# Kernel tuning notes

Hardware: AMD Instinct MI355X
Metric: run time of the kernel (lower is better)

The kernel has to match this reference:

```python
import jax, jax.numpy as jnp
import numpy as np

IN_DIM = 3
N_FEATS = 8
HASHMAP_SIZE = 524288
RESOLUTION = 128.0
PRIMES = np.array([1, 2654435761, 805459861], dtype=np.uint32)
# bin_mask[n, d] = (n & (1 << d)) == 0, for the 2^d corner offsets
_neigh = np.arange(1 << IN_DIM, dtype=np.int64).reshape(-1, 1)
_dims = np.arange(IN_DIM, dtype=np.int64).reshape(1, -1)
BIN_MASK = (_neigh & (1 << _dims)) == 0  # [8, 3] bool


def setup_inputs() -> dict:
    key = jax.random.key(0)
    k1, k2 = jax.random.split(key)
    x = jax.random.uniform(k1, (2000000, IN_DIM), dtype=jnp.float32)
    emb = jax.random.normal(k2, (HASHMAP_SIZE, N_FEATS), dtype=jnp.float32) * 0.1
    return {"x": x, "emb": emb}


def _hash(idx_u32, primes_u32):
    # idx_u32: [..., d] uint32; multiply wraps mod 2^32 (== & 0xFFFFFFFF), xor-reduce dims
    p = idx_u32 * primes_u32  # uint32 wraparound
    h = p[..., 0]
    for i in range(1, p.shape[-1]):
        h = h ^ p[..., i]
    return (h % jnp.uint32(HASHMAP_SIZE)).astype(jnp.int32)


def reference(x, emb):
    primes = jnp.asarray(PRIMES)
    bin_mask = jnp.asarray(BIN_MASK)  # [8, 3]
    xr = x * RESOLUTION                      # [N, 3]
    xi = jnp.floor(xr)                       # [N, 3] float (long() on positive coords)
    xf = xr - xi                             # fractional part; grad == identity (detach on xi)
    xi_u = xi.astype(jnp.uint32)
    # corner integer coords: [N, 8, 3]
    idx = jnp.where(bin_mask[None, :, :], xi_u[:, None, :], xi_u[:, None, :] + jnp.uint32(1))
    # trilinear weights: [N, 8]
    w = jnp.prod(jnp.where(bin_mask[None, :, :], 1.0 - xf[:, None, :], xf[:, None, :]), axis=-1)
    hash_ids = _hash(idx, primes)            # [N, 8] int32
    feats = emb[hash_ids]                    # [N, 8, F]
    return jnp.sum(feats * w[..., None], axis=-2)  # [N, F]
```

## Files before the change

kernel.cpp:

```cpp
#include <hip/hip_runtime.h>


#define HASHMAP_SIZE 524288
#define HASHMAP_MASK 524287u
#define RESOLUTION   128.0f
#define PRIME1       2654435761u
#define PRIME2       805459861u

typedef float f32x4 __attribute__((ext_vector_type(4)));
typedef int   i32x2 __attribute__((ext_vector_type(2)));
typedef int   i32x4 __attribute__((ext_vector_type(4)));

#define NRED_BLOCKS 256

__global__ __launch_bounds__(256) void absmax_stage1(
    const float* __restrict__ emb, float* __restrict__ blockmax)
{
    __shared__ float smax[256];
    int tid = threadIdx.x;
    int stride = gridDim.x * blockDim.x;
    const float4* e4 = reinterpret_cast<const float4*>(emb);
    const int total4 = HASHMAP_SIZE * 2;
    float m = 0.f;
    for (int idx = blockIdx.x * blockDim.x + tid; idx < total4; idx += stride) {
        float4 v = e4[idx];
        m = fmaxf(m, fmaxf(fmaxf(fabsf(v.x), fabsf(v.y)),
                           fmaxf(fabsf(v.z), fabsf(v.w))));
    }
    smax[tid] = m;
    __syncthreads();
    for (int s = 128; s > 0; s >>= 1) {
        if (tid < s) smax[tid] = fmaxf(smax[tid], smax[tid + s]);
        __syncthreads();
    }
    if (tid == 0) blockmax[blockIdx.x] = smax[0];
}

__global__ __launch_bounds__(256) void quantize_fused(
    const float* __restrict__ emb, const float* __restrict__ blockmax,
    i32x2* __restrict__ tab, float* __restrict__ scale)
{
    __shared__ float smax[256];
    int tid = threadIdx.x;
    smax[tid] = blockmax[tid];
    __syncthreads();
    for (int s = 128; s > 0; s >>= 1) {
        if (tid < s) smax[tid] = fmaxf(smax[tid], smax[tid + s]);
        __syncthreads();
    }
    float sc = (smax[0] > 0.f) ? smax[0] : 1.0f;
    if (blockIdx.x == 0 && tid == 0) scale[0] = sc;

    int r = blockIdx.x * blockDim.x + tid;
    if (r >= HASHMAP_SIZE) return;
    float rs = 127.0f / sc;
    const float4* src = reinterpret_cast<const float4*>(emb) + 2 * r;
    float4 lo = src[0];
    float4 hi = src[1];
    int b0 = __float2int_rn(lo.x * rs), b1 = __float2int_rn(lo.y * rs);
    int b2 = __float2int_rn(lo.z * rs), b3 = __float2int_rn(lo.w * rs);
    int b4 = __float2int_rn(hi.x * rs), b5 = __float2int_rn(hi.y * rs);
    int b6 = __float2int_rn(hi.z * rs), b7 = __float2int_rn(hi.w * rs);
    i32x2 o;
    o.x = (int)((b0 & 0xff) | ((b1 & 0xff) << 8) |
                ((b2 & 0xff) << 16) | ((unsigned)b3 << 24));
    o.y = (int)((b4 & 0xff) | ((b5 & 0xff) << 8) |
                ((b6 & 0xff) << 16) | ((unsigned)b7 << 24));
    tab[r] = o;
}

__device__ __forceinline__ float sb(int v, int sh) {
    return (float)((int)((unsigned)v << (24 - sh)) >> 24);
}

__global__ __launch_bounds__(256) void hashgrid_i8_kernel(
    const float* __restrict__ x,
    const i32x2* __restrict__ tab,
    const float* __restrict__ scale,
    float* __restrict__ out,
    int n)
{
    int i = blockIdx.x * blockDim.x + threadIdx.x;
    if (i >= n) return;

    float x0 = __builtin_nontemporal_load(x + 3 * i + 0);
    float x1 = __builtin_nontemporal_load(x + 3 * i + 1);
    float x2 = __builtin_nontemporal_load(x + 3 * i + 2);

    float xr0 = x0 * RESOLUTION;
    float xr1 = x1 * RESOLUTION;
    float xr2 = x2 * RESOLUTION;

    float fl0 = floorf(xr0);
    float fl1 = floorf(xr1);
    float fl2 = floorf(xr2);

    float f0 = xr0 - fl0;
    float f1 = xr1 - fl1;
    float f2 = xr2 - fl2;

    unsigned u0 = (unsigned)(int)fl0;
    unsigned u1 = (unsigned)(int)fl1;
    unsigned u2 = (unsigned)(int)fl2;

    unsigned h1a = u1 * PRIME1, h1b = (u1 + 1u) * PRIME1;
    unsigned h2a = u2 * PRIME2, h2b = (u2 + 1u) * PRIME2;

    bool even = ((u0 & 1u) == 0u);

    i32x2 qv[8];
    i32x4 pv[4];
    unsigned rl[4];
    if (even) {
#pragma unroll
        for (int cp = 0; cp < 4; ++cp) {
            unsigned t1 = (cp & 1) ? h1b : h1a;
            unsigned t2 = (cp & 2) ? h2b : h2a;
            unsigned r  = (u0 ^ t1 ^ t2) & HASHMAP_MASK;
            rl[cp] = r;
            const i32x2* p = tab + (r & ~1u);
            asm volatile("global_load_dwordx4 %0, %1, off"
                         : "=&v"(pv[cp]) : "v"(p));
        }
    } else {
#pragma unroll
        for (int c = 0; c < 8; ++c) {
            unsigned t0 = (c & 1) ? (u0 + 1u) : u0;
            unsigned t1 = (c & 2) ? h1b : h1a;
            unsigned t2 = (c & 4) ? h2b : h2a;
            unsigned r  = (t0 ^ t1 ^ t2) & HASHMAP_MASK;
            const i32x2* p = tab + r;
            asm volatile("global_load_dwordx2 %0, %1, off"
                         : "=&v"(qv[c]) : "v"(p));
        }
    }
    asm volatile("s_waitcnt vmcnt(0)" ::: "memory");
    __builtin_amdgcn_sched_barrier(0);

    if (even) {
#pragma unroll
        for (int cp = 0; cp < 4; ++cp) {
            bool swap = (rl[cp] & 1u) != 0u;
            i32x2 lo; lo.x = pv[cp].x; lo.y = pv[cp].y;
            i32x2 hi; hi.x = pv[cp].z; hi.y = pv[cp].w;
            qv[2 * cp + 0] = swap ? hi : lo;
            qv[2 * cp + 1] = swap ? lo : hi;
        }
    }

    float g0 = 1.0f - f0;
    float g1 = 1.0f - f1;
    float g2 = 1.0f - f2;

    float acc0 = 0.f, acc1 = 0.f, acc2 = 0.f, acc3 = 0.f;
    float acc4 = 0.f, acc5 = 0.f, acc6 = 0.f, acc7 = 0.f;

#pragma unroll
    for (int cp = 0; cp < 4; ++cp) {
        float w12 = ((cp & 1) ? f1 : g1) * ((cp & 2) ? f2 : g2);
#pragma unroll
        for (int c0 = 0; c0 < 2; ++c0) {
            float w = w12 * (c0 ? f0 : g0);
            int a = qv[2 * cp + c0].x, b = qv[2 * cp + c0].y;
            acc0 += w * sb(a, 0);  acc1 += w * sb(a, 8);
            acc2 += w * sb(a, 16); acc3 += w * sb(a, 24);
            acc4 += w * sb(b, 0);  acc5 += w * sb(b, 8);
            acc6 += w * sb(b, 16); acc7 += w * sb(b, 24);
        }
    }

    float os = scale[0] * (1.0f / 127.0f);
    f32x4* o = reinterpret_cast<f32x4*>(out) + (size_t)i * 2u;
    f32x4 o0 = {acc0 * os, acc1 * os, acc2 * os, acc3 * os};
    f32x4 o1 = {acc4 * os, acc5 * os, acc6 * os, acc7 * os};
    __builtin_nontemporal_store(o0, o);
    __builtin_nontemporal_store(o1, o + 1);
}

__global__ __launch_bounds__(256) void hashgrid_fp32_kernel(
    const float* __restrict__ x,
    const float* __restrict__ emb,
    float* __restrict__ out,
    int n)
{
    int i = blockIdx.x * blockDim.x + threadIdx.x;
    if (i >= n) return;

    float x0 = x[i * 3 + 0], x1 = x[i * 3 + 1], x2 = x[i * 3 + 2];
    float xr0 = x0 * RESOLUTION, xr1 = x1 * RESOLUTION, xr2 = x2 * RESOLUTION;
    float fl0 = floorf(xr0), fl1 = floorf(xr1), fl2 = floorf(xr2);
    float f0 = xr0 - fl0, f1 = xr1 - fl1, f2 = xr2 - fl2;
    unsigned u0 = (unsigned)(int)fl0, u1 = (unsigned)(int)fl1, u2 = (unsigned)(int)fl2;

    unsigned h0a = u0,          h0b = u0 + 1u;
    unsigned h1a = u1 * PRIME1, h1b = (u1 + 1u) * PRIME1;
    unsigned h2a = u2 * PRIME2, h2b = (u2 + 1u) * PRIME2;

    float g0 = 1.0f - f0, g1 = 1.0f - f1, g2 = 1.0f - f2;
    float acc0 = 0.f, acc1 = 0.f, acc2 = 0.f, acc3 = 0.f;
    float acc4 = 0.f, acc5 = 0.f, acc6 = 0.f, acc7 = 0.f;

#pragma unroll
    for (int c = 0; c < 8; ++c) {
        unsigned h = (((c & 1) ? h0b : h0a) ^
                      ((c & 2) ? h1b : h1a) ^
                      ((c & 4) ? h2b : h2a)) & HASHMAP_MASK;
        float w = ((c & 1) ? f0 : g0) *
                  ((c & 2) ? f1 : g1) *
                  ((c & 4) ? f2 : g2);
        const float4* e = reinterpret_cast<const float4*>(emb) + (h << 1);
        float4 e0 = e[0];
        float4 e1 = e[1];
        acc0 += w * e0.x; acc1 += w * e0.y; acc2 += w * e0.z; acc3 += w * e0.w;
        acc4 += w * e1.x; acc5 += w * e1.y; acc6 += w * e1.z; acc7 += w * e1.w;
    }

    float4* o = reinterpret_cast<float4*>(out) + (size_t)i * 2u;
    o[0] = make_float4(acc0, acc1, acc2, acc3);
    o[1] = make_float4(acc4, acc5, acc6, acc7);
}

extern "C" void kernel_launch(void* const* d_in, const int* in_sizes, int n_in,
                              void* d_out, int out_size, void* d_ws, size_t ws_size,
                              hipStream_t stream) {
    const float* x   = (const float*)d_in[0];
    const float* emb = (const float*)d_in[1];
    float* out = (float*)d_out;

    int n = in_sizes[0] / 3;
    int block = 256;
    int grid = (n + block - 1) / block;

    size_t tab_bytes   = (size_t)HASHMAP_SIZE * 8u;
    size_t bm_off      = tab_bytes;
    size_t scale_off   = tab_bytes + NRED_BLOCKS * sizeof(float);
    size_t need        = scale_off + sizeof(float);

    if (ws_size >= need) {
        i32x2* tab      = (i32x2*)d_ws;
        float* blockmax = (float*)((char*)d_ws + bm_off);
        float* scale    = (float*)((char*)d_ws + scale_off);

        absmax_stage1<<<NRED_BLOCKS, 256, 0, stream>>>(emb, blockmax);
        int qgrid = (HASHMAP_SIZE + block - 1) / block;
        quantize_fused<<<qgrid, block, 0, stream>>>(emb, blockmax, tab, scale);
        hashgrid_i8_kernel<<<grid, block, 0, stream>>>(x, tab, scale, out, n);
    } else {
        hashgrid_fp32_kernel<<<grid, block, 0, stream>>>(x, emb, out, n);
    }
}
```

Baseline: 78.05 us.

## Stage x loads through LDS and unify gather path for odd/even corners

```diff
diff --git a/kernel.cpp b/kernel.cpp
--- a/kernel.cpp
+++ b/kernel.cpp
@@ -80,12 +80,26 @@
     float* __restrict__ out,
     int n)
 {
-    int i = blockIdx.x * blockDim.x + threadIdx.x;
-    if (i >= n) return;
-
-    float x0 = __builtin_nontemporal_load(x + 3 * i + 0);
-    float x1 = __builtin_nontemporal_load(x + 3 * i + 1);
-    float x2 = __builtin_nontemporal_load(x + 3 * i + 2);
+    __shared__ float xs[768];
+    int tid = threadIdx.x;
+    int i = blockIdx.x * 256 + tid;
+    bool valid = (i < n);
+
+    {
+        int base = blockIdx.x * 768;
+        int lim = n * 3;
+#pragma unroll
+        for (int k = 0; k < 3; ++k) {
+            int g = base + k * 256 + tid;
+            xs[k * 256 + tid] = (g < lim) ? __builtin_nontemporal_load(x + g) : 0.f;
+        }
+    }
+    __syncthreads();
+    if (!valid) return;
+
+    float x0 = xs[3 * tid + 0];
+    float x1 = xs[3 * tid + 1];
+    float x2 = xs[3 * tid + 2];
 
     float xr0 = x0 * RESOLUTION;
     float xr1 = x1 * RESOLUTION;
@@ -108,43 +122,24 @@
 
     bool even = ((u0 & 1u) == 0u);
 
-    i32x2 qv[8];
     i32x4 pv[4];
-    unsigned rl[4];
-    if (even) {
+    i32x2 qb[4] = {};
+    unsigned ra[4];
+#pragma unroll
+    for (int cp = 0; cp < 4; ++cp) {
+        unsigned mm = ((cp & 1) ? h1b : h1a) ^ ((cp & 2) ? h2b : h2a);
+        unsigned r  = (u0 ^ mm) & HASHMAP_MASK;
+        ra[cp] = r;
+        const i32x4* p = reinterpret_cast<const i32x4*>(
+            reinterpret_cast<const char*>(tab) + (size_t)(r & ~1u) * 8u);
+        pv[cp] = *p;
+    }
+    if (!even) {
 #pragma unroll
         for (int cp = 0; cp < 4; ++cp) {
-            unsigned t1 = (cp & 1) ? h1b : h1a;
-            unsigned t2 = (cp & 2) ? h2b : h2a;
-            unsigned r  = (u0 ^ t1 ^ t2) & HASHMAP_MASK;
-            rl[cp] = r;
-            const i32x2* p = tab + (r & ~1u);
-            asm volatile("global_load_dwordx4 %0, %1, off"
-                         : "=&v"(pv[cp]) : "v"(p));
-        }
-    } else {
-#pragma unroll
-        for (int c = 0; c < 8; ++c) {
-            unsigned t0 = (c & 1) ? (u0 + 1u) : u0;
-            unsigned t1 = (c & 2) ? h1b : h1a;
-            unsigned t2 = (c & 4) ? h2b : h2a;
-            unsigned r  = (t0 ^ t1 ^ t2) & HASHMAP_MASK;
-            const i32x2* p = tab + r;
-            asm volatile("global_load_dwordx2 %0, %1, off"
-                         : "=&v"(qv[c]) : "v"(p));
-        }
-    }
-    asm volatile("s_waitcnt vmcnt(0)" ::: "memory");
-    __builtin_amdgcn_sched_barrier(0);
-
-    if (even) {
-#pragma unroll
-        for (int cp = 0; cp < 4; ++cp) {
-            bool swap = (rl[cp] & 1u) != 0u;
-            i32x2 lo; lo.x = pv[cp].x; lo.y = pv[cp].y;
-            i32x2 hi; hi.x = pv[cp].z; hi.y = pv[cp].w;
-            qv[2 * cp + 0] = swap ? hi : lo;
-            qv[2 * cp + 1] = swap ? lo : hi;
+            unsigned mm = ((cp & 1) ? h1b : h1a) ^ ((cp & 2) ? h2b : h2a);
+            unsigned rb = ((u0 + 1u) ^ mm) & HASHMAP_MASK;
+            qb[cp] = tab[rb];
         }
     }
 
@@ -158,15 +153,24 @@
 #pragma unroll
     for (int cp = 0; cp < 4; ++cp) {
         float w12 = ((cp & 1) ? f1 : g1) * ((cp & 2) ? f2 : g2);
-#pragma unroll
-        for (int c0 = 0; c0 < 2; ++c0) {
-            float w = w12 * (c0 ? f0 : g0);
-            int a = qv[2 * cp + c0].x, b = qv[2 * cp + c0].y;
-            acc0 += w * sb(a, 0);  acc1 += w * sb(a, 8);
-            acc2 += w * sb(a, 16); acc3 += w * sb(a, 24);
-            acc4 += w * sb(b, 0);  acc5 += w * sb(b, 8);
-            acc6 += w * sb(b, 16); acc7 += w * sb(b, 24);
-        }
+        bool hiA = (ra[cp] & 1u) != 0u;
+        int lox = pv[cp].x, loy = pv[cp].y;
+        int hix = pv[cp].z, hiy = pv[cp].w;
+        int cAx = hiA ? hix : lox, cAy = hiA ? hiy : loy;
+        int cOx = hiA ? lox : hix, cOy = hiA ? loy : hiy;
+        int cBx = even ? cOx : qb[cp].x;
+        int cBy = even ? cOy : qb[cp].y;
+
+        float wA = w12 * g0;
+        float wB = w12 * f0;
+        acc0 += wA * sb(cAx, 0)  + wB * sb(cBx, 0);
+        acc1 += wA * sb(cAx, 8)  + wB * sb(cBx, 8);
+        acc2 += wA * sb(cAx, 16) + wB * sb(cBx, 16);
+        acc3 += wA * sb(cAx, 24) + wB * sb(cBx, 24);
+        acc4 += wA * sb(cAy, 0)  + wB * sb(cBy, 0);
+        acc5 += wA * sb(cAy, 8)  + wB * sb(cBy, 8);
+        acc6 += wA * sb(cAy, 16) + wB * sb(cBy, 16);
+        acc7 += wA * sb(cAy, 24) + wB * sb(cBy, 24);
     }
 
     float os = scale[0] * (1.0f / 127.0f);
```

Measured after the change: 82.78 us (median of 2 runs). 1.06x slower.

## Fuse absmax reduction and int8 quantization into one cooperative grid-sync kernel

Applied to the files above, without the earlier changes.

```diff
diff --git a/kernel.cpp b/kernel.cpp
--- a/kernel.cpp
+++ b/kernel.cpp
@@ -1,4 +1,7 @@
 #include <hip/hip_runtime.h>
+#include <hip/hip_cooperative_groups.h>
+
+namespace cg = cooperative_groups;
 
 
 #define HASHMAP_SIZE 524288
@@ -12,6 +15,62 @@
 typedef int   i32x4 __attribute__((ext_vector_type(4)));
 
 #define NRED_BLOCKS 256
+#define PREP_BLOCKS 1024
+
+__device__ __forceinline__ int pack4(float4 v, float rs) {
+    int b0 = __float2int_rn(v.x * rs), b1 = __float2int_rn(v.y * rs);
+    int b2 = __float2int_rn(v.z * rs), b3 = __float2int_rn(v.w * rs);
+    return (int)((b0 & 0xff) | ((b1 & 0xff) << 8) |
+                 ((b2 & 0xff) << 16) | ((unsigned)b3 << 24));
+}
+
+__global__ __launch_bounds__(256) void prep_coop(
+    const float* __restrict__ emb,
+    i32x2* __restrict__ tab,
+    unsigned* __restrict__ scale_u,
+    float* __restrict__ scalef)
+{
+    int t = blockIdx.x * 256 + threadIdx.x;
+    const float4* e4 = reinterpret_cast<const float4*>(emb);
+    float4 v0 = e4[4 * t + 0];
+    float4 v1 = e4[4 * t + 1];
+    float4 v2 = e4[4 * t + 2];
+    float4 v3 = e4[4 * t + 3];
+
+    float m = fabsf(v0.x);
+    m = fmaxf(m, fabsf(v0.y)); m = fmaxf(m, fabsf(v0.z)); m = fmaxf(m, fabsf(v0.w));
+    m = fmaxf(m, fabsf(v1.x)); m = fmaxf(m, fabsf(v1.y));
+    m = fmaxf(m, fabsf(v1.z)); m = fmaxf(m, fabsf(v1.w));
+    m = fmaxf(m, fabsf(v2.x)); m = fmaxf(m, fabsf(v2.y));
+    m = fmaxf(m, fabsf(v2.z)); m = fmaxf(m, fabsf(v2.w));
+    m = fmaxf(m, fabsf(v3.x)); m = fmaxf(m, fabsf(v3.y));
+    m = fmaxf(m, fabsf(v3.z)); m = fmaxf(m, fabsf(v3.w));
+
+    __shared__ float sm[256];
+    sm[threadIdx.x] = m;
+    __syncthreads();
+    for (int s = 128; s > 0; s >>= 1) {
+        if (threadIdx.x < s) sm[threadIdx.x] = fmaxf(sm[threadIdx.x], sm[threadIdx.x + s]);
+        __syncthreads();
+    }
+    if (threadIdx.x == 0) atomicMax(scale_u, __float_as_uint(sm[0]));
+
+    cg::this_grid().sync();
+
+    unsigned su = __hip_atomic_load(scale_u, __ATOMIC_RELAXED,
+                                    __HIP_MEMORY_SCOPE_AGENT);
+    float sc = __uint_as_float(su);
+    if (!(sc > 0.f)) sc = 1.0f;
+    if (t == 0) scalef[0] = sc;
+
+    float rs = 127.0f / sc;
+    i32x4 o;
+    o.x = pack4(v0, rs);
+    o.y = pack4(v1, rs);
+    o.z = pack4(v2, rs);
+    o.w = pack4(v3, rs);
+    *reinterpret_cast<i32x4*>(&tab[2 * t]) = o;
+}
 
 __global__ __launch_bounds__(256) void absmax_stage1(
     const float* __restrict__ emb, float* __restrict__ blockmax)
@@ -38,7 +97,7 @@
 
 __global__ __launch_bounds__(256) void quantize_fused(
     const float* __restrict__ emb, const float* __restrict__ blockmax,
-    i32x2* __restrict__ tab, float* __restrict__ scale)
+    i32x2* __restrict__ tab, float* __restrict__ scalef)
 {
     __shared__ float smax[256];
     int tid = threadIdx.x;
@@ -49,23 +108,15 @@
         __syncthreads();
     }
     float sc = (smax[0] > 0.f) ? smax[0] : 1.0f;
-    if (blockIdx.x == 0 && tid == 0) scale[0] = sc;
+    if (blockIdx.x == 0 && tid == 0) scalef[0] = sc;
 
     int r = blockIdx.x * blockDim.x + tid;
     if (r >= HASHMAP_SIZE) return;
     float rs = 127.0f / sc;
     const float4* src = reinterpret_cast<const float4*>(emb) + 2 * r;
-    float4 lo = src[0];
-    float4 hi = src[1];
-    int b0 = __float2int_rn(lo.x * rs), b1 = __float2int_rn(lo.y * rs);
-    int b2 = __float2int_rn(lo.z * rs), b3 = __float2int_rn(lo.w * rs);
-    int b4 = __float2int_rn(hi.x * rs), b5 = __float2int_rn(hi.y * rs);
-    int b6 = __float2int_rn(hi.z * rs), b7 = __float2int_rn(hi.w * rs);
     i32x2 o;
-    o.x = (int)((b0 & 0xff) | ((b1 & 0xff) << 8) |
-                ((b2 & 0xff) << 16) | ((unsigned)b3 << 24));
-    o.y = (int)((b4 & 0xff) | ((b5 & 0xff) << 8) |
-                ((b6 & 0xff) << 16) | ((unsigned)b7 << 24));
+    o.x = pack4(src[0], rs);
+    o.y = pack4(src[1], rs);
     tab[r] = o;
 }
 
@@ -231,20 +282,33 @@
     int block = 256;
     int grid = (n + block - 1) / block;
 
-    size_t tab_bytes   = (size_t)HASHMAP_SIZE * 8u;
-    size_t bm_off      = tab_bytes;
-    size_t scale_off   = tab_bytes + NRED_BLOCKS * sizeof(float);
-    size_t need        = scale_off + sizeof(float);
+    size_t tab_bytes = (size_t)HASHMAP_SIZE * 8u;
+    size_t su_off    = tab_bytes;
+    size_t sf_off    = tab_bytes + 16;
+    size_t bm_off    = tab_bytes + 64;
+    size_t need      = bm_off + NRED_BLOCKS * sizeof(float);
 
     if (ws_size >= need) {
-        i32x2* tab      = (i32x2*)d_ws;
-        float* blockmax = (float*)((char*)d_ws + bm_off);
-        float* scale    = (float*)((char*)d_ws + scale_off);
-
-        absmax_stage1<<<NRED_BLOCKS, 256, 0, stream>>>(emb, blockmax);
-        int qgrid = (HASHMAP_SIZE + block - 1) / block;
-        quantize_fused<<<qgrid, block, 0, stream>>>(emb, blockmax, tab, scale);
-        hashgrid_i8_kernel<<<grid, block, 0, stream>>>(x, tab, scale, out, n);
+        i32x2*    tab      = (i32x2*)d_ws;
+        unsigned* scale_u  = (unsigned*)((char*)d_ws + su_off);
+        float*    scalef   = (float*)((char*)d_ws + sf_off);
+        float*    blockmax = (float*)((char*)d_ws + bm_off);
+
+        hipMemsetAsync(scale_u, 0, sizeof(unsigned), stream);
+
+        const float* emb_p = emb;
+        i32x2* tab_p = tab;
+        unsigned* su_p = scale_u;
+        float* sf_p = scalef;
+        void* args[] = { (void*)&emb_p, (void*)&tab_p, (void*)&su_p, (void*)&sf_p };
+        hipError_t e = hipLaunchCooperativeKernel(
+            (const void*)prep_coop, dim3(PREP_BLOCKS), dim3(256), args, 0, stream);
+        if (e != hipSuccess) {
+            absmax_stage1<<<NRED_BLOCKS, 256, 0, stream>>>(emb, blockmax);
+            int qgrid = (HASHMAP_SIZE + block - 1) / block;
+            quantize_fused<<<qgrid, block, 0, stream>>>(emb, blockmax, tab, scalef);
+        }
+        hashgrid_i8_kernel<<<grid, block, 0, stream>>>(x, tab, scalef, out, n);
     } else {
         hashgrid_fp32_kernel<<<grid, block, 0, stream>>>(x, emb, out, n);
     }
```

Measured after the change: 133.9 us. +71.6%, slower.
